# Optimization experiments

Measured on AMD Instinct MI355X. Metric: run time of the kernel, lower is better.

The kernel has to match this reference:

```python
import jax, jax.numpy as jnp
import numpy as np

BATCH = 32768
FEAT_DIM = 2048
NUM_CLASSES = 3


def setup_inputs() -> dict:
    key = jax.random.key(0)
    k1, k2, k3 = jax.random.split(key, 3)
    feat = jax.random.normal(k1, (BATCH, FEAT_DIM), dtype=jnp.float32)
    label = jax.random.randint(k2, (BATCH,), 0, NUM_CLASSES, dtype=jnp.int64)
    centers = jax.random.normal(k3, (NUM_CLASSES, FEAT_DIM), dtype=jnp.float32)
    return {"feat": feat, "label": label, "centers": centers}


def reference(feat, label, centers):
    # feat: [B, D], label: [B] in {0,1,2}, centers: [3, D]
    batch_size = feat.shape[0]
    lab = label.astype(jnp.int32)
    # gather own center and the two "other" centers (vectorized form of the
    # original python loop: for label l the other classes are (l+1)%3, (l+2)%3)
    centers_batch = centers[lab]              # [B, D]
    centers_batch1 = centers[(lab + 1) % 3]   # [B, D]
    centers_batch2 = centers[(lab + 2) % 3]   # [B, D]
    distocen = jnp.sum((feat - centers_batch1) ** 2) + jnp.sum((feat - centers_batch2) ** 2)
    main = jnp.sum((feat - centers_batch) ** 2)
    loss = main * (1.0 + 1.0 / distocen) / 2.0 / batch_size
    return loss
```

## Files before the change

kernel.cpp:

```cpp
#include <hip/hip_runtime.h>


constexpr int BATCH = 32768;
constexpr int FEAT = 2048;
constexpr int FEAT4 = FEAT / 4;
constexpr int BLOCKS = 2048;
constexpr int TPB = 256;

__global__ __launch_bounds__(TPB) void cl_main_kernel(
    const float4* __restrict__ feat4,
    const int* __restrict__ label,
    const float4* __restrict__ cent4,
    float* __restrict__ accum)
{
    const int total = BATCH * FEAT4;
    int idx = blockIdx.x * TPB + threadIdx.x;
    const int stride = gridDim.x * TPB;

    float m_acc = 0.f;
    float t_acc = 0.f;

    for (; idx < total; idx += stride) {
        const int b = idx >> 9;
        const int d = idx & 511;
        const float4 f  = feat4[idx];
        const float4 c0 = cent4[d];
        const float4 c1 = cent4[FEAT4 + d];
        const float4 c2 = cent4[2 * FEAT4 + d];
        const int l = label[b];

        float ex, ey, ez, ew;
        ex = f.x - c0.x; ey = f.y - c0.y; ez = f.z - c0.z; ew = f.w - c0.w;
        const float s0 = ex*ex + ey*ey + ez*ez + ew*ew;
        ex = f.x - c1.x; ey = f.y - c1.y; ez = f.z - c1.z; ew = f.w - c1.w;
        const float s1 = ex*ex + ey*ey + ez*ez + ew*ew;
        ex = f.x - c2.x; ey = f.y - c2.y; ez = f.z - c2.z; ew = f.w - c2.w;
        const float s2 = ex*ex + ey*ey + ez*ez + ew*ew;

        t_acc += s0 + s1 + s2;
        const float sm = (l == 0) ? s0 : ((l == 1) ? s1 : s2);
        m_acc += sm;
    }

    #pragma unroll
    for (int off = 32; off > 0; off >>= 1) {
        m_acc += __shfl_down(m_acc, off, 64);
        t_acc += __shfl_down(t_acc, off, 64);
    }

    __shared__ float sm_red[TPB / 64];
    __shared__ float st_red[TPB / 64];
    const int wave = threadIdx.x >> 6;
    const int lane = threadIdx.x & 63;
    if (lane == 0) { sm_red[wave] = m_acc; st_red[wave] = t_acc; }
    __syncthreads();
    if (threadIdx.x == 0) {
        float M = 0.f, T = 0.f;
        #pragma unroll
        for (int w = 0; w < TPB / 64; ++w) { M += sm_red[w]; T += st_red[w]; }
        atomicAdd(&accum[0], M);
        atomicAdd(&accum[1], T);
    }
}

__global__ void cl_final_kernel(const float* __restrict__ accum,
                                float* __restrict__ out)
{
    const float m = accum[0];
    const float dist = accum[1] - m;
    out[0] = m * (1.0f + 1.0f / dist) * 0.5f / (float)BATCH;
}

extern "C" void kernel_launch(void* const* d_in, const int* in_sizes, int n_in,
                              void* d_out, int out_size, void* d_ws, size_t ws_size,
                              hipStream_t stream) {
    const float4* feat    = (const float4*)d_in[0];
    const int*    label   = (const int*)d_in[1];
    const float4* centers = (const float4*)d_in[2];
    float* out   = (float*)d_out;
    float* accum = (float*)d_ws;

    hipMemsetAsync(accum, 0, 2 * sizeof(float), stream);
    cl_main_kernel<<<BLOCKS, TPB, 0, stream>>>(feat, label, centers, accum);
    cl_final_kernel<<<1, 1, 0, stream>>>(accum, out);
}
```

Baseline: 373.7 us.

## Assign rows per block with register-resident centers and staged labels

Restructures the main kernel so each block processes a contiguous set of rows and each thread handles one fixed feature column. The three center vectors are loaded once into registers and the block's labels are staged in shared memory, removing the repeated center and label loads from the inner loop. Feature loads use nontemporal hints and the loop is unrolled. The trade-off is a fixed grid that depends on the batch dividing evenly, plus a barrier at kernel start.

```diff
diff --git a/kernel.cpp b/kernel.cpp
--- a/kernel.cpp
+++ b/kernel.cpp
@@ -1,45 +1,48 @@
 #include <hip/hip_runtime.h>
 
 
-constexpr int BATCH = 32768;
-constexpr int FEAT = 2048;
-constexpr int FEAT4 = FEAT / 4;
-constexpr int BLOCKS = 2048;
-constexpr int TPB = 256;
+typedef float fvec4 __attribute__((ext_vector_type(4)));
+
+constexpr int BATCH  = 32768;
+constexpr int FEAT4  = 512;
+constexpr int TPB    = 512;
+constexpr int BLOCKS = 1024;
+constexpr int ROWS   = BATCH / BLOCKS;
 
 __global__ __launch_bounds__(TPB) void cl_main_kernel(
-    const float4* __restrict__ feat4,
+    const fvec4* __restrict__ feat4,
     const int* __restrict__ label,
-    const float4* __restrict__ cent4,
+    const fvec4* __restrict__ cent4,
     float* __restrict__ accum)
 {
-    const int total = BATCH * FEAT4;
-    int idx = blockIdx.x * TPB + threadIdx.x;
-    const int stride = gridDim.x * TPB;
+    const int d = threadIdx.x;
 
-    float m_acc = 0.f;
-    float t_acc = 0.f;
+    const fvec4 c0 = cent4[d];
+    const fvec4 c1 = cent4[FEAT4 + d];
+    const fvec4 c2 = cent4[2 * FEAT4 + d];
 
-    for (; idx < total; idx += stride) {
-        const int b = idx >> 9;
-        const int d = idx & 511;
-        const float4 f  = feat4[idx];
-        const float4 c0 = cent4[d];
-        const float4 c1 = cent4[FEAT4 + d];
-        const float4 c2 = cent4[2 * FEAT4 + d];
-        const int l = label[b];
+    __shared__ int slab[ROWS];
+    const int b0 = blockIdx.x * ROWS;
+    if (threadIdx.x < ROWS) slab[threadIdx.x] = label[b0 + threadIdx.x];
+    __syncthreads();
 
-        float ex, ey, ez, ew;
-        ex = f.x - c0.x; ey = f.y - c0.y; ez = f.z - c0.z; ew = f.w - c0.w;
-        const float s0 = ex*ex + ey*ey + ez*ez + ew*ew;
-        ex = f.x - c1.x; ey = f.y - c1.y; ez = f.z - c1.z; ew = f.w - c1.w;
-        const float s1 = ex*ex + ey*ey + ez*ez + ew*ew;
-        ex = f.x - c2.x; ey = f.y - c2.y; ez = f.z - c2.z; ew = f.w - c2.w;
-        const float s2 = ex*ex + ey*ey + ez*ez + ew*ew;
+    float m_acc = 0.f, t_acc = 0.f;
+    const fvec4* fp = feat4 + (size_t)b0 * FEAT4 + d;
+
+    #pragma unroll 4
+    for (int r = 0; r < ROWS; ++r) {
+        const fvec4 f = __builtin_nontemporal_load(&fp[(size_t)r * FEAT4]);
+        const int l = slab[r];
+
+        fvec4 e0 = f - c0;
+        fvec4 e1 = f - c1;
+        fvec4 e2 = f - c2;
+        const float s0 = e0.x*e0.x + e0.y*e0.y + e0.z*e0.z + e0.w*e0.w;
+        const float s1 = e1.x*e1.x + e1.y*e1.y + e1.z*e1.z + e1.w*e1.w;
+        const float s2 = e2.x*e2.x + e2.y*e2.y + e2.z*e2.z + e2.w*e2.w;
 
         t_acc += s0 + s1 + s2;
-        const float sm = (l == 0) ? s0 : ((l == 1) ? s1 : s2);
-        m_acc += sm;
+        m_acc += (l == 0) ? s0 : ((l == 1) ? s1 : s2);
     }
 
     #pragma unroll
@@ -74,13 +77,13 @@
 extern "C" void kernel_launch(void* const* d_in, const int* in_sizes, int n_in,
                               void* d_out, int out_size, void* d_ws, size_t ws_size,
                               hipStream_t stream) {
-    const float4* feat    = (const float4*)d_in[0];
-    const int*    label   = (const int*)d_in[1];
-    const float4* centers = (const float4*)d_in[2];
+    const fvec4* feat    = (const fvec4*)d_in[0];
+    const int*   label   = (const int*)d_in[1];
+    const fvec4* centers = (const fvec4*)d_in[2];
     float* out   = (float*)d_out;
     float* accum = (float*)d_ws;
 
-    hipMemsetAsync(accum, 0, 2 * sizeof(float), stream);
+    (void)hipMemsetAsync(accum, 0, 2 * sizeof(float), stream);
     cl_main_kernel<<<BLOCKS, TPB, 0, stream>>>(feat, label, centers, accum);
     cl_final_kernel<<<1, 1, 0, stream>>>(accum, out);
 }
```

New measurement: 347.1 us. 1.08x faster.
